# Kernel optimization log

Measured on AMD Instinct MI355X. Metric: run time of the kernel, lower is better.

The kernel has to match this reference:

```python
import jax, jax.numpy as jnp
import numpy as np

N = 100000      # nodes
E = 1600000     # edges (avg degree 16)
D_IN = 128
D_OUT = 128
P = 0.5         # dropout prob (module is in training mode)


def setup_inputs() -> dict:
    key = jax.random.key(0)
    k1, k2, k3 = jax.random.split(key, 3)
    x = jax.random.normal(k1, (N, D_IN), dtype=jnp.float32)
    edge_index = jax.random.randint(k2, (2, E), 0, N, dtype=jnp.int32)
    # GCNConv learned params (glorot-ish weight, zero bias)
    weight = jax.random.normal(k3, (D_IN, D_OUT), dtype=jnp.float32) / np.float32(np.sqrt(D_IN))
    bias = jnp.zeros((D_OUT,), dtype=jnp.float32)
    return {"x": x, "edge_index": edge_index, "weight": weight, "bias": bias}


def reference(x, edge_index, weight, bias):
    # --- GCNConv: add self-loops, symmetric deg^-1/2 normalization ---
    loops = jnp.arange(N, dtype=edge_index.dtype)
    src = jnp.concatenate([edge_index[0], loops])   # [E+N]
    dst = jnp.concatenate([edge_index[1], loops])   # [E+N]
    deg = jax.ops.segment_sum(jnp.ones_like(dst, dtype=x.dtype), dst, num_segments=N)
    dinv = jnp.where(deg > 0, jax.lax.rsqrt(deg), 0.0)          # deg^-1/2
    norm = dinv[src] * dinv[dst]                                # [E+N]
    h = x @ weight                                              # [N, D_OUT]
    msgs = h[src] * norm[:, None]                               # gather + scale
    out = jax.ops.segment_sum(msgs, dst, num_segments=N) + bias # scatter-add
    # --- ReLU ---
    out = jax.nn.relu(out)
    # --- Dropout (training=True), fixed key for determinism ---
    keep = jax.random.bernoulli(jax.random.key(42), 1.0 - P, out.shape)
    return jnp.where(keep, out / (1.0 - P), jnp.zeros((), out.dtype))
```

## Files before the change

### kernel.cpp

```cpp
#include <hip/hip_runtime.h>

#define N_NODES 100000
#define E_EDGES 1600000
#define D 128
#define PAD 136
#define GEMM_BLKS 1563
#define SCHUNK 4096
#define SCAT_BLKS ((E_EDGES + SCHUNK - 1) / SCHUNK)
#define RANGE 98
#define NR 1024
#define RCAP 2048
#define CAP 2048
#define NPW 13

typedef __attribute__((ext_vector_type(8))) short short8;
typedef __attribute__((ext_vector_type(8))) unsigned short ushort8v;
typedef __attribute__((ext_vector_type(4))) float f32x4;

__device__ __forceinline__ unsigned int rotl32(unsigned int x, int r) {
  return (x << r) | (x >> (32 - r));
}

__device__ __forceinline__ unsigned int threefry_bits(unsigned int ctr) {
  const unsigned int ks0 = 0u, ks1 = 42u;
  const unsigned int ks2 = ks0 ^ ks1 ^ 0x1BD11BDAu;
  unsigned int x0 = ks0;
  unsigned int x1 = ctr + ks1;
#define TF_ROUND(R) { x0 += x1; x1 = rotl32(x1, R); x1 ^= x0; }
  TF_ROUND(13) TF_ROUND(15) TF_ROUND(26) TF_ROUND(6)
  x0 += ks1; x1 += ks2 + 1u;
  TF_ROUND(17) TF_ROUND(29) TF_ROUND(16) TF_ROUND(24)
  x0 += ks2; x1 += ks0 + 2u;
  TF_ROUND(13) TF_ROUND(15) TF_ROUND(26) TF_ROUND(6)
  x0 += ks0; x1 += ks1 + 3u;
  TF_ROUND(17) TF_ROUND(29) TF_ROUND(16) TF_ROUND(24)
  x0 += ks1; x1 += ks2 + 4u;
  TF_ROUND(13) TF_ROUND(15) TF_ROUND(26) TF_ROUND(6)
  x0 += ks2; x1 += ks0 + 5u;
#undef TF_ROUND
  return x0 ^ x1;
}

__device__ __forceinline__ unsigned short f2bf(float f) {
  unsigned int u = __float_as_uint(f);
  u = (u + 0x7FFFu + ((u >> 16) & 1u)) >> 16;
  return (unsigned short)u;
}
__device__ __forceinline__ float bf2f_lo(unsigned int v) {
  return __uint_as_float(v << 16);
}
__device__ __forceinline__ float bf2f_hi(unsigned int v) {
  return __uint_as_float(v & 0xFFFF0000u);
}

__global__ __launch_bounds__(256) void k_init(const float* __restrict__ w,
                                              unsigned short* __restrict__ wbf,
                                              int* __restrict__ cur) {
  int t = blockIdx.x * 256 + threadIdx.x;
  int k = t >> 7;
  int n = t & 127;
  wbf[n * 128 + k] = f2bf(w[t]);
  if (t < NR) cur[t] = t * RCAP;
}

__global__ __launch_bounds__(256) void k_scat(const int* __restrict__ ei,
                                              int* __restrict__ cur,
                                              int* __restrict__ ebuf) {
  __shared__ int lcnt[NR];
  __shared__ int gb[NR];
  __shared__ int sc2[NR];
  const int t = threadIdx.x;
  const int e0 = blockIdx.x * SCHUNK;
  for (int i = t; i < NR; i += 256) { lcnt[i] = 0; sc2[i] = 0; }
  __syncthreads();
  int myd[SCHUNK / 256];
#pragma unroll
  for (int i = 0; i < SCHUNK / 256; ++i) {
    int e = e0 + i * 256 + t;
    myd[i] = -1;
    if (e < E_EDGES) {
      int d = ei[E_EDGES + e];
      myd[i] = d;
      atomicAdd(&lcnt[d / RANGE], 1);
    }
  }
  __syncthreads();
  for (int i = t; i < NR; i += 256) {
    int c = lcnt[i];
    gb[i] = c ? atomicAdd(&cur[i], c) : 0;
  }
  __syncthreads();
#pragma unroll
  for (int i = 0; i < SCHUNK / 256; ++i) {
    int d = myd[i];
    if (d >= 0) {
      int e = e0 + i * 256 + t;
      int s = ei[e];
      int b = d / RANGE;
      int dl = d - b * RANGE;
      int pos = gb[b] + atomicAdd(&sc2[b], 1);
      if (pos < (b + 1) * RCAP)
        ebuf[pos] = s | (dl << 17);
    }
  }
}

__global__ __launch_bounds__(256) void k_deg(const int* __restrict__ ebuf,
                                             const int* __restrict__ cur,
                                             float* __restrict__ dinv) {
  __shared__ int hist[128];
  const int t = threadIdx.x;
  const int r = blockIdx.x;
  if (t < 128) hist[t] = 0;
  __syncthreads();
  const int lo = r * RCAP;
  const int hi = min(cur[r], lo + RCAP);
  for (int e = lo + t; e < hi; e += 256)
    atomicAdd(&hist[((unsigned)ebuf[e]) >> 17], 1);
  __syncthreads();
  if (t < RANGE) {
    int n = r * RANGE + t;
    if (n < N_NODES) dinv[n] = rsqrtf((float)(hist[t] + 1));
  }
}

__global__ __launch_bounds__(256) void k_gemm(const float* __restrict__ x,
                                              const unsigned short* __restrict__ wbf,
                                              unsigned short* __restrict__ h) {
  __shared__ unsigned short Wl[128 * PAD];
  __shared__ unsigned short Xl[64 * PAD];
  const int t = threadIdx.x;
  const int row0 = blockIdx.x * 64;

#pragma unroll
  for (int i = 0; i < 8; ++i) {
    int u  = t + i * 256;
    int kg = u & 15;
    int n  = u >> 4;
    *(ushort8v*)&Wl[n * PAD + kg * 8] = *(const ushort8v*)&wbf[n * 128 + kg * 8];
  }
  const float4* x4 = (const float4*)x;
#pragma unroll
  for (int i = 0; i < 8; ++i) {
    int id = t + i * 256;
    int r  = id >> 5;
    int c4 = id & 31;
    int row = row0 + r; if (row >= N_NODES) row = N_NODES - 1;
    float4 v = x4[(long long)row * 32 + c4];
    ushort4 p;
    p.x = f2bf(v.x); p.y = f2bf(v.y); p.z = f2bf(v.z); p.w = f2bf(v.w);
    *(ushort4*)&Xl[r * PAD + c4 * 4] = p;
  }
  __syncthreads();

  const int wv   = t >> 6;
  const int l    = t & 63;
  const int quad = l >> 4;
  const int ln16 = l & 15;
  const int m0   = wv * 16;

  short8 a[4];
#pragma unroll
  for (int kt = 0; kt < 4; ++kt)
    a[kt] = *(const short8*)&Xl[(m0 + ln16) * PAD + kt * 32 + quad * 8];

#pragma unroll
  for (int nt = 0; nt < 8; ++nt) {
    f32x4 acc = {0.f, 0.f, 0.f, 0.f};
#pragma unroll
    for (int kt = 0; kt < 4; ++kt) {
      short8 b = *(const short8*)&Wl[(nt * 16 + ln16) * PAD + kt * 32 + quad * 8];
      acc = __builtin_amdgcn_mfma_f32_16x16x32_bf16(a[kt], b, acc, 0, 0, 0);
    }
#pragma unroll
    for (int r = 0; r < 4; ++r)
      Xl[(m0 + quad * 4 + r) * PAD + nt * 16 + ln16] = f2bf(acc[r]);
  }

#pragma unroll
  for (int v = 0; v < 4; ++v) {
    int idx = v * 64 + l;
    int rr  = idx >> 4;
    int ch  = idx & 15;
    int row = row0 + m0 + rr;
    if (row < N_NODES)
      *(ushort8v*)&h[(long long)row * D + ch * 8] = *(const ushort8v*)&Xl[(m0 + rr) * PAD + ch * 8];
  }
}

__global__ __launch_bounds__(512) void k_agg(const int* __restrict__ ebuf,
                                             const int* __restrict__ cur,
                                             const float* __restrict__ dinv,
                                             const unsigned short* __restrict__ h,
                                             const float* __restrict__ bias,
                                             float* __restrict__ out) {
  __shared__ int ssort[CAP];
  __shared__ int shist[128];
  __shared__ int sscn[128];
  __shared__ int scur[128];
  const int t  = threadIdx.x;
  const int r  = blockIdx.x;
  const int wv = t >> 6;
  const int l  = t & 63;
  const unsigned int* h32 = (const unsigned int*)h;

  float a0[NPW], a1[NPW];
#pragma unroll
  for (int j = 0; j < NPW; ++j) { a0[j] = 0.f; a1[j] = 0.f; }

  const int lo = r * RCAP;
  const int m  = min(cur[r], lo + RCAP) - lo;

  if (t < 128) shist[t] = 0;
  __syncthreads();

  int pk0 = -1, pk1 = -1, pk2 = -1, pk3 = -1;
  {
    int i0 = t, i1 = t + 512, i2 = t + 1024, i3 = t + 1536;
    if (i0 < m) { pk0 = ebuf[lo + i0]; atomicAdd(&shist[((unsigned)pk0) >> 17], 1); }
    if (i1 < m) { pk1 = ebuf[lo + i1]; atomicAdd(&shist[((unsigned)pk1) >> 17], 1); }
    if (i2 < m) { pk2 = ebuf[lo + i2]; atomicAdd(&shist[((unsigned)pk2) >> 17], 1); }
    if (i3 < m) { pk3 = ebuf[lo + i3]; atomicAdd(&shist[((unsigned)pk3) >> 17], 1); }
  }
  __syncthreads();

  if (t < 128) sscn[t] = shist[t];
  __syncthreads();
  for (int off = 1; off < 128; off <<= 1) {
    int xv = (t < 128 && t >= off) ? sscn[t - off] : 0;
    __syncthreads();
    if (t < 128) sscn[t] += xv;
    __syncthreads();
  }
  if (t < 128) scur[t] = sscn[t] - shist[t];
  __syncthreads();

  if (pk0 != -1) ssort[atomicAdd(&scur[((unsigned)pk0) >> 17], 1)] = pk0 & 0x1FFFF;
  if (pk1 != -1) ssort[atomicAdd(&scur[((unsigned)pk1) >> 17], 1)] = pk1 & 0x1FFFF;
  if (pk2 != -1) ssort[atomicAdd(&scur[((unsigned)pk2) >> 17], 1)] = pk2 & 0x1FFFF;
  if (pk3 != -1) ssort[atomicAdd(&scur[((unsigned)pk3) >> 17], 1)] = pk3 & 0x1FFFF;
  __syncthreads();

#pragma unroll
  for (int j = 0; j < NPW; ++j) {
    int nl = wv + 8 * j;
    if (nl < RANGE) {
      int s1i = sscn[nl];
      int s0i = s1i - shist[nl];
      float aa0 = a0[j], aa1 = a1[j];
#pragma unroll 4
      for (int e = s0i; e < s1i; ++e) {
        int s = ssort[e];
        float wgt = dinv[s];
        unsigned u = h32[(long long)s * 64 + l];
        aa0 = fmaf(bf2f_lo(u), wgt, aa0);
        aa1 = fmaf(bf2f_hi(u), wgt, aa1);
      }
      a0[j] = aa0; a1[j] = aa1;
    }
  }

#pragma unroll
  for (int j = 0; j < NPW; ++j) {
    int nl = wv + 8 * j;
    if (nl >= RANGE) continue;
    int n = r * RANGE + nl;
    if (n >= N_NODES) continue;
    float dv = rsqrtf((float)(shist[nl] + 1));
    unsigned hv = h32[(long long)n * 64 + l];
    float v0 = (a0[j] + bf2f_lo(hv) * dv) * dv;
    float v1 = (a1[j] + bf2f_hi(hv) * dv) * dv;
    float2 bb = ((const float2*)bias)[l];
    float r0 = fmaxf(v0 + bb.x, 0.f);
    float r1 = fmaxf(v1 + bb.y, 0.f);
    unsigned i0 = (unsigned)n * 128u + (unsigned)(2 * l);
    unsigned b0 = threefry_bits(i0);
    unsigned b1 = threefry_bits(i0 + 1u);
    float2 res;
    res.x = (b0 & 0x80000000u) ? 0.0f : r0 * 2.0f;
    res.y = (b1 & 0x80000000u) ? 0.0f : r1 * 2.0f;
    ((float2*)out)[(long long)n * 64 + l] = res;
  }
}

extern "C" void kernel_launch(void* const* d_in, const int* in_sizes, int n_in,
                              void* d_out, int out_size, void* d_ws, size_t ws_size,
                              hipStream_t stream) {
  const float* x    = (const float*)d_in[0];
  const int*   ei   = (const int*)d_in[1];
  const float* w    = (const float*)d_in[2];
  const float* bias = (const float*)d_in[3];
  float* out = (float*)d_out;

  char* p = (char*)d_ws;
  unsigned short* h   = (unsigned short*)p;  p += (size_t)N_NODES * D * 2;
  unsigned short* wbf = (unsigned short*)p;  p += 128 * 128 * 2;
  float* dinv = (float*)p;                   p += (size_t)(NR * RANGE) * 4;
  int* cur    = (int*)p;                     p += NR * 4;
  int* ebuf   = (int*)p;                     p += (size_t)NR * RCAP * 4;

  k_init<<<64, 256, 0, stream>>>(w, wbf, cur);
  k_scat<<<SCAT_BLKS, 256, 0, stream>>>(ei, cur, ebuf);
  k_deg<<<NR, 256, 0, stream>>>(ebuf, cur, dinv);
  k_gemm<<<GEMM_BLKS, 256, 0, stream>>>(x, wbf, h);
  k_agg<<<NR, 512, 0, stream>>>(ebuf, cur, dinv, h, bias, out);
}
```

Before: 225.0 us.

## Sort edges by source octant and accumulate via fixed-point LDS atomics

Edges in each destination range are now bucketed by which eighth of the source-node space they come from, with a per-thread salt, instead of by destination node. Each block walks the octants starting from a block-dependent offset, so concurrently running blocks gather h rows from the same region and L2 locality should improve. Because edges are no longer grouped by destination, per-node accumulation moves from registers to shared-memory integer atomics on a fixed-point scale. This adds LDS atomic traffic, quantization error and a possible overflow risk in the fixed-point sums. The epilogue now reads dinv[n] from memory instead of recomputing it from the local histogram.

```diff
diff --git a/kernel.cpp b/kernel.cpp
--- a/kernel.cpp
+++ b/kernel.cpp
@@ -11,7 +11,9 @@
 #define NR 1024
 #define RCAP 2048
 #define CAP 2048
-#define NPW 13
+#define OCTN 12500
+#define SCALE_F 524288.0f
+#define INV_SC (1.0f / 524288.0f)
 
 typedef __attribute__((ext_vector_type(8))) short short8;
 typedef __attribute__((ext_vector_type(8))) unsigned short ushort8v;
@@ -195,6 +197,7 @@
                                              const float* __restrict__ bias,
                                              float* __restrict__ out) {
   __shared__ int ssort[CAP];
+  __shared__ int accI[RANGE * 128];
   __shared__ int shist[128];
   __shared__ int sscn[128];
   __shared__ int scur[128];
@@ -202,25 +205,25 @@
   const int r  = blockIdx.x;
   const int wv = t >> 6;
   const int l  = t & 63;
+  const int ostart = r & 7;
   const unsigned int* h32 = (const unsigned int*)h;
-
-  float a0[NPW], a1[NPW];
-#pragma unroll
-  for (int j = 0; j < NPW; ++j) { a0[j] = 0.f; a1[j] = 0.f; }
 
   const int lo = r * RCAP;
   const int m  = min(cur[r], lo + RCAP) - lo;
 
+  for (int i = t; i < RANGE * 128; i += 512) accI[i] = 0;
   if (t < 128) shist[t] = 0;
   __syncthreads();
 
   int pk0 = -1, pk1 = -1, pk2 = -1, pk3 = -1;
+  int bk0 = 0, bk1 = 0, bk2 = 0, bk3 = 0;
+  const int salt = (t & 15);
   {
     int i0 = t, i1 = t + 512, i2 = t + 1024, i3 = t + 1536;
-    if (i0 < m) { pk0 = ebuf[lo + i0]; atomicAdd(&shist[((unsigned)pk0) >> 17], 1); }
-    if (i1 < m) { pk1 = ebuf[lo + i1]; atomicAdd(&shist[((unsigned)pk1) >> 17], 1); }
-    if (i2 < m) { pk2 = ebuf[lo + i2]; atomicAdd(&shist[((unsigned)pk2) >> 17], 1); }
-    if (i3 < m) { pk3 = ebuf[lo + i3]; atomicAdd(&shist[((unsigned)pk3) >> 17], 1); }
+    if (i0 < m) { pk0 = ebuf[lo + i0]; bk0 = (((pk0 & 0x1FFFF) / OCTN) << 4) | salt; atomicAdd(&shist[bk0], 1); }
+    if (i1 < m) { pk1 = ebuf[lo + i1]; bk1 = (((pk1 & 0x1FFFF) / OCTN) << 4) | salt; atomicAdd(&shist[bk1], 1); }
+    if (i2 < m) { pk2 = ebuf[lo + i2]; bk2 = (((pk2 & 0x1FFFF) / OCTN) << 4) | salt; atomicAdd(&shist[bk2], 1); }
+    if (i3 < m) { pk3 = ebuf[lo + i3]; bk3 = (((pk3 & 0x1FFFF) / OCTN) << 4) | salt; atomicAdd(&shist[bk3], 1); }
   }
   __syncthreads();
 
@@ -235,51 +238,50 @@
   if (t < 128) scur[t] = sscn[t] - shist[t];
   __syncthreads();
 
-  if (pk0 != -1) ssort[atomicAdd(&scur[((unsigned)pk0) >> 17], 1)] = pk0 & 0x1FFFF;
-  if (pk1 != -1) ssort[atomicAdd(&scur[((unsigned)pk1) >> 17], 1)] = pk1 & 0x1FFFF;
-  if (pk2 != -1) ssort[atomicAdd(&scur[((unsigned)pk2) >> 17], 1)] = pk2 & 0x1FFFF;
-  if (pk3 != -1) ssort[atomicAdd(&scur[((unsigned)pk3) >> 17], 1)] = pk3 & 0x1FFFF;
-  __syncthreads();
-
-#pragma unroll
-  for (int j = 0; j < NPW; ++j) {
-    int nl = wv + 8 * j;
-    if (nl < RANGE) {
-      int s1i = sscn[nl];
-      int s0i = s1i - shist[nl];
-      float aa0 = a0[j], aa1 = a1[j];
-#pragma unroll 4
-      for (int e = s0i; e < s1i; ++e) {
-        int s = ssort[e];
-        float wgt = dinv[s];
-        unsigned u = h32[(long long)s * 64 + l];
-        aa0 = fmaf(bf2f_lo(u), wgt, aa0);
-        aa1 = fmaf(bf2f_hi(u), wgt, aa1);
-      }
-      a0[j] = aa0; a1[j] = aa1;
+  if (pk0 != -1) ssort[atomicAdd(&scur[bk0], 1)] = pk0;
+  if (pk1 != -1) ssort[atomicAdd(&scur[bk1], 1)] = pk1;
+  if (pk2 != -1) ssort[atomicAdd(&scur[bk2], 1)] = pk2;
+  if (pk3 != -1) ssort[atomicAdd(&scur[bk3], 1)] = pk3;
+  __syncthreads();
+
+  for (int op = 0; op < 8; ++op) {
+    int oct = (ostart + op) & 7;
+    int b0  = oct << 4;
+    int s0i = (b0 == 0) ? 0 : sscn[b0 - 1];
+    int s1i = sscn[b0 + 15];
+    for (int e = s0i + wv; e < s1i; e += 8) {
+      int p  = ssort[e];
+      int s  = p & 0x1FFFF;
+      int dl = ((unsigned)p) >> 17;
+      float ws = dinv[s] * SCALE_F;
+      unsigned u = h32[(long long)s * 64 + l];
+      int v0 = __float2int_rn(bf2f_lo(u) * ws);
+      int v1 = __float2int_rn(bf2f_hi(u) * ws);
+      atomicAdd(&accI[dl * 128 + l], v0);
+      atomicAdd(&accI[dl * 128 + 64 + l], v1);
     }
   }
-
-#pragma unroll
-  for (int j = 0; j < NPW; ++j) {
-    int nl = wv + 8 * j;
-    if (nl >= RANGE) continue;
-    int n = r * RANGE + nl;
+  __syncthreads();
+
+  for (int u4 = t; u4 < RANGE * 64; u4 += 512) {
+    int nl = u4 >> 6;
+    int p  = u4 & 63;
+    int n  = r * RANGE + nl;
     if (n >= N_NODES) continue;
-    float dv = rsqrtf((float)(shist[nl] + 1));
-    unsigned hv = h32[(long long)n * 64 + l];
-    float v0 = (a0[j] + bf2f_lo(hv) * dv) * dv;
-    float v1 = (a1[j] + bf2f_hi(hv) * dv) * dv;
-    float2 bb = ((const float2*)bias)[l];
+    float dv = dinv[n];
+    unsigned hv = h32[(long long)n * 64 + p];
+    float v0 = (accI[nl * 128 + p] * INV_SC + bf2f_lo(hv) * dv) * dv;
+    float v1 = (accI[nl * 128 + 64 + p] * INV_SC + bf2f_hi(hv) * dv) * dv;
+    float2 bb = ((const float2*)bias)[p];
     float r0 = fmaxf(v0 + bb.x, 0.f);
     float r1 = fmaxf(v1 + bb.y, 0.f);
-    unsigned i0 = (unsigned)n * 128u + (unsigned)(2 * l);
+    unsigned i0 = (unsigned)n * 128u + (unsigned)(2 * p);
     unsigned b0 = threefry_bits(i0);
     unsigned b1 = threefry_bits(i0 + 1u);
     float2 res;
     res.x = (b0 & 0x80000000u) ? 0.0f : r0 * 2.0f;
     res.y = (b1 & 0x80000000u) ? 0.0f : r1 * 2.0f;
-    ((float2*)out)[(long long)n * 64 + l] = res;
+    ((float2*)out)[(long long)n * 64 + p] = res;
   }
 }
 
```

Measured after the change: 327.6 us. +45.6%, slower.
